# Performance work log

Hardware: AMD Instinct MI355X
Metric: run time of the kernel (lower is better)

The kernel has to match this reference:

```python
import jax, jax.numpy as jnp
import numpy as np

C = 128        # in_channels
HEADS = 4      # n_heads
GROUPS = 32    # GroupNorm groups
EPS = 1e-6
B, H, W = 1, 64, 64


def setup_inputs() -> dict:
    key = jax.random.key(0)
    ks = jax.random.split(key, 5)
    def w(k):
        return jax.random.normal(k, (C, C), jnp.float32) * 0.02
    return {
        "x": jax.random.normal(ks[0], (B, C, H, W), jnp.float32),
        "gn_gamma": jnp.ones((C,), jnp.float32),
        "gn_beta": jnp.zeros((C,), jnp.float32),
        "wq": w(ks[1]), "bq": jnp.zeros((C,), jnp.float32),
        "wk": w(ks[2]), "bk": jnp.zeros((C,), jnp.float32),
        "wv": w(ks[3]), "bv": jnp.zeros((C,), jnp.float32),
        "wp": w(ks[4]), "bp": jnp.zeros((C,), jnp.float32),
    }


def _group_norm(x, gamma, beta):
    b, c, h, w = x.shape
    xg = x.reshape(b, GROUPS, c // GROUPS, h, w)
    mu = xg.mean(axis=(2, 3, 4), keepdims=True)
    var = xg.var(axis=(2, 3, 4), keepdims=True)
    xn = ((xg - mu) * jax.lax.rsqrt(var + EPS)).reshape(b, c, h, w)
    return xn * gamma[None, :, None, None] + beta[None, :, None, None]


def _conv1x1(x, wgt, bias):
    # 1x1 conv == per-pixel channel matmul
    return jnp.einsum('bchw,oc->bohw', x, wgt) + bias[None, :, None, None]


def reference(x, gn_gamma, gn_beta, wq, bq, wk, bk, wv, bv, wp, bp):
    b, c, h, w = x.shape
    cph = c // HEADS  # channels per head
    xn = _group_norm(x, gn_gamma, gn_beta)
    q = _conv1x1(xn, wq, bq)
    k = _conv1x1(xn, wk, bk)
    v = _conv1x1(xn, wv, bv)

    # einops 'b (c heads) h w': heads is the INNER channel factor
    def split_ch(t):  # -> (b, heads, cph, h*w)
        return t.reshape(b, cph, HEADS, h * w).transpose(0, 2, 1, 3)

    qh = split_ch(q).transpose(0, 1, 3, 2)  # (b, heads, hw, cph)
    kh = split_ch(k)                          # (b, heads, cph, hw)
    vh = split_ch(v)                          # (b, heads, cph, hw)

    scale = c ** (-0.5)  # NOTE: full in_channels, as in the original code
    attn = jnp.einsum('bhic,bhcj->bhij', qh, kh) * scale  # (b, heads, hw, hw)
    attn = jax.nn.softmax(attn, axis=2)  # softmax over QUERY axis (dim=2), non-standard

    out = jnp.einsum('bhik,bhjk->bhji', attn, vh)  # (b, heads, cph, hw)
    # 'b heads c (h w) -> b (c heads) h w'
    out = out.reshape(b, HEADS, cph, h, w).transpose(0, 2, 1, 3, 4).reshape(b, c, h, w)
    return _conv1x1(out, wp, bp) + x
```

## Files before the change

### kernel.cpp

```cpp
#include <hip/hip_runtime.h>
#include <hip/hip_bf16.h>


#define HWSZ 4096
#define QSCALE2 0.12752649759422368f
#define QSPLIT 8
#define KSPLIT 8
#define EPS 1e-6f

typedef __bf16 bf16x8 __attribute__((ext_vector_type(8)));
typedef float f32x4 __attribute__((ext_vector_type(4)));

union FragU { uint4 u; bf16x8 v; };

#if __has_builtin(__builtin_amdgcn_exp2f)
#define EXP2F(x) __builtin_amdgcn_exp2f(x)
#else
#define EXP2F(x) exp2f(x)
#endif

__device__ __forceinline__ unsigned int pack_bf16(float lo, float hi) {
  unsigned int ul, uh;
  __builtin_memcpy(&ul, &lo, 4);
  __builtin_memcpy(&uh, &hi, 4);
  return __builtin_amdgcn_perm(uh + 0x8000u, ul + 0x8000u, 0x07060302u);
}

__global__ __launch_bounds__(256) void prep_kernel(
    const float* __restrict__ wq, const float* __restrict__ wk,
    const float* __restrict__ wv, const float* __restrict__ wp,
    const float* __restrict__ x, __hip_bfloat16* __restrict__ wb,
    float* __restrict__ gnpart) {
  int b = blockIdx.x, t = threadIdx.x;
  if (b < 64) {
    int m = b >> 4, chunk = b & 15;
    const float* src = (m == 0) ? wq : (m == 1) ? wk : (m == 2) ? wv : wp;
    float sc = (m == 0) ? QSCALE2 : 1.0f;
    int idx = chunk * 1024 + t * 4;
    float4 v = *reinterpret_cast<const float4*>(src + idx);
    uint2 st;
    st.x = pack_bf16(v.x * sc, v.y * sc);
    st.y = pack_bf16(v.z * sc, v.w * sc);
    *reinterpret_cast<uint2*>(wb + m * 16384 + idx) = st;
  } else {
    int ch = b - 64;
    const float4* x4 = reinterpret_cast<const float4*>(x + ch * HWSZ);
    float s = 0.f, ss = 0.f;
    for (int e = t; e < 1024; e += 256) {
      float4 v = x4[e];
      s += v.x + v.y + v.z + v.w;
      ss += v.x * v.x + v.y * v.y + v.z * v.z + v.w * v.w;
    }
    for (int off = 32; off; off >>= 1) {
      s += __shfl_down(s, off);
      ss += __shfl_down(ss, off);
    }
    __shared__ float rs[4], rss[4];
    int wid = t >> 6;
    if ((t & 63) == 0) { rs[wid] = s; rss[wid] = ss; }
    __syncthreads();
    if (t == 0) {
      gnpart[ch] = rs[0] + rs[1] + rs[2] + rs[3];
      gnpart[128 + ch] = rss[0] + rss[1] + rss[2] + rss[3];
    }
  }
}

__global__ __launch_bounds__(512) void qkv_mfma_kernel(
    const float* __restrict__ x, const float* __restrict__ gnpart,
    const float* __restrict__ gamma, const float* __restrict__ beta,
    const __hip_bfloat16* __restrict__ wb, const float* __restrict__ bq,
    const float* __restrict__ bk, const float* __restrict__ bv,
    __hip_bfloat16* __restrict__ qt, __hip_bfloat16* __restrict__ kt,
    __hip_bfloat16* __restrict__ vb) {
  __shared__ float stats_lds[32][2];
  __shared__ __align__(16) __hip_bfloat16 xnT[16][136];
  __shared__ __align__(16) __hip_bfloat16 qs_[4][16][40];
  __shared__ __align__(16) __hip_bfloat16 ks_[4][16][40];
  __shared__ __align__(16) __hip_bfloat16 vs_[128][24];
  int t = threadIdx.x;
  int p0 = blockIdx.x * 16;
  if (t < 32) {
    float s = 0.f, ss = 0.f;
#pragma unroll
    for (int q = 0; q < 4; ++q) {
      s += gnpart[t * 4 + q];
      ss += gnpart[128 + t * 4 + q];
    }
    float mu = s * (1.f / 16384.f);
    float var = ss * (1.f / 16384.f) - mu * mu;
    stats_lds[t][0] = mu;
    stats_lds[t][1] = rsqrtf(var + EPS);
  }
  __syncthreads();
#pragma unroll
  for (int e = t; e < 2048; e += 512) {
    int c = e >> 4, p = e & 15;
    int g = c >> 2;
    float xv = x[c * HWSZ + p0 + p];
    float xn = (xv - stats_lds[g][0]) * stats_lds[g][1] * gamma[c] + beta[c];
    xnT[p][c] = __float2bfloat16(xn);
  }
  __syncthreads();
  int lane = t & 63, w = t >> 6;
  int l15 = lane & 15, g = lane >> 4;
  FragU bfr[4];
#pragma unroll
  for (int kk = 0; kk < 4; ++kk)
    bfr[kk].u = *reinterpret_cast<const uint4*>(&xnT[l15][kk * 32 + 8 * g]);
  int o0 = w * 16;

#define DO_CONV(WMAT, BIAS, BSCALE, LDSW)                                        \
  {                                                                              \
    f32x4 bi = *reinterpret_cast<const f32x4*>((BIAS) + o0 + 4 * g);             \
    f32x4 acc = bi * (BSCALE);                                                   \
    _Pragma("unroll") for (int kk = 0; kk < 4; ++kk) {                           \
      FragU a;                                                                   \
      a.u = *reinterpret_cast<const uint4*>((WMAT) +                             \
            (o0 + l15) * 128 + kk * 32 + 8 * g);                                 \
      acc = __builtin_amdgcn_mfma_f32_16x16x32_bf16(a.v, bfr[kk].v, acc, 0, 0, 0); \
    }                                                                            \
    _Pragma("unroll") for (int r = 0; r < 4; ++r) {                              \
      int o = o0 + 4 * g + r;                                                    \
      LDSW;                                                                      \
    }                                                                            \
  }

  DO_CONV(wb, bq, QSCALE2, qs_[o & 3][l15][o >> 2] = __float2bfloat16(acc[r]))
  DO_CONV(wb + 16384, bk, 1.0f, ks_[o & 3][l15][o >> 2] = __float2bfloat16(acc[r]))
  DO_CONV(wb + 32768, bv, 1.0f, vs_[o][l15] = __float2bfloat16(acc[r]))
#undef DO_CONV
  __syncthreads();
  if (t < 256) {
    int row = t >> 2, ch = t & 3;
    int h = row >> 4, p = row & 15;
    uint4 vq = *reinterpret_cast<const uint4*>(&qs_[h][p][ch * 8]);
    *reinterpret_cast<uint4*>(qt + (h * HWSZ + p0 + p) * 32 + ch * 8) = vq;
  } else {
    int tt = t - 256;
    int row = tt >> 2, ch = tt & 3;
    int h = row >> 4, p = row & 15;
    uint4 vk = *reinterpret_cast<const uint4*>(&ks_[h][p][ch * 8]);
    *reinterpret_cast<uint4*>(kt + (h * HWSZ + p0 + p) * 32 + ch * 8) = vk;
  }
  if (t < 256) {
    int o = t >> 1, half = t & 1;
    uint4 vv = *reinterpret_cast<const uint4*>(&vs_[o][half * 8]);
    *reinterpret_cast<uint4*>(vb + o * HWSZ + p0 + half * 8) = vv;
  }
}

__global__ __launch_bounds__(256, 4) void colstats_kernel(
    const __hip_bfloat16* __restrict__ qt, const __hip_bfloat16* __restrict__ kt,
    float* __restrict__ colpart) {
  int h = blockIdx.y, t = threadIdx.x, qs = blockIdx.z;
  int w = t >> 6, lane = t & 63;
  int l15 = lane & 15, g = lane >> 4;
  int k0 = blockIdx.x * 256 + w * 64;
  FragU a[4];
#pragma unroll
  for (int u = 0; u < 4; ++u)
    a[u].u = *reinterpret_cast<const uint4*>(kt + (h * HWSZ + k0 + u * 16 + l15) * 32 + 8 * g);
  float l[4][4];
#pragma unroll
  for (int u = 0; u < 4; ++u)
#pragma unroll
    for (int r = 0; r < 4; ++r) l[u][r] = 0.f;
  const __hip_bfloat16* qbase =
      qt + h * HWSZ * 32 + (qs * (HWSZ / QSPLIT) + l15) * 32 + 8 * g;
  f32x4 z = {0.f, 0.f, 0.f, 0.f};
#pragma unroll 2
  for (int it = 0; it < HWSZ / QSPLIT / 16; ++it) {
    FragU b;
    b.u = *reinterpret_cast<const uint4*>(qbase + it * 512);
#pragma unroll
    for (int u = 0; u < 4; ++u) {
      f32x4 d = __builtin_amdgcn_mfma_f32_16x16x32_bf16(a[u].v, b.v, z, 0, 0, 0);
#pragma unroll
      for (int r = 0; r < 4; ++r) l[u][r] += EXP2F(d[r]);
    }
  }
#pragma unroll
  for (int off = 1; off < 16; off <<= 1)
#pragma unroll
    for (int u = 0; u < 4; ++u)
#pragma unroll
      for (int r = 0; r < 4; ++r) l[u][r] += __shfl_xor(l[u][r], off);
  if (l15 == 0) {
#pragma unroll
    for (int u = 0; u < 4; ++u)
#pragma unroll
      for (int r = 0; r < 4; ++r)
        colpart[(qs * 4 + h) * HWSZ + k0 + u * 16 + 4 * g + r] = l[u][r];
  }
}

__global__ __launch_bounds__(256) void wscale_kernel(
    const float* __restrict__ colpart, __hip_bfloat16* __restrict__ vb) {
  __shared__ float rlds[128];
  int b = blockIdx.x, t = threadIdx.x;
  int kr0 = b * 32;
  if (t < 128) {
    int h = t >> 5, k = kr0 + (t & 31);
    float s = 0.f;
#pragma unroll
    for (int qs = 0; qs < QSPLIT; ++qs) s += colpart[(qs * 4 + h) * HWSZ + k];
    rlds[t] = 1.0f / s;
  }
  __syncthreads();
  int row = t >> 1, koff = (t & 1) * 16;
  int h = row & 3;
  __hip_bfloat16* p = vb + row * HWSZ + kr0 + koff;
  FragU u0, u1;
  u0.u = *reinterpret_cast<const uint4*>(p);
  u1.u = *reinterpret_cast<const uint4*>(p + 8);
  const float* r = rlds + h * 32 + koff;
  float f[16];
#pragma unroll
  for (int j = 0; j < 8; ++j) {
    f[j] = (float)u0.v[j] * r[j];
    f[8 + j] = (float)u1.v[j] * r[8 + j];
  }
  uint4 s0, s1;
  s0.x = pack_bf16(f[0], f[1]);  s0.y = pack_bf16(f[2], f[3]);
  s0.z = pack_bf16(f[4], f[5]);  s0.w = pack_bf16(f[6], f[7]);
  s1.x = pack_bf16(f[8], f[9]);  s1.y = pack_bf16(f[10], f[11]);
  s1.z = pack_bf16(f[12], f[13]); s1.w = pack_bf16(f[14], f[15]);
  *reinterpret_cast<uint4*>(p) = s0;
  *reinterpret_cast<uint4*>(p + 8) = s1;
}

__global__ __launch_bounds__(256, 4) void attn_pv_kernel(
    const __hip_bfloat16* __restrict__ qt, const __hip_bfloat16* __restrict__ kt,
    const __hip_bfloat16* __restrict__ vb, __hip_bfloat16* __restrict__ aopb) {
  __shared__ __align__(16) char p_lds[4][2][2048];
  int h = blockIdx.y, t = threadIdx.x;
  int kc0 = blockIdx.z * (HWSZ / KSPLIT);
  int w = t >> 6, lane = t & 63;
  int l15 = lane & 15, g = lane >> 4;
  int swz = l15 & 7;
  int i0 = blockIdx.x * 128 + w * 32;
  FragU bq0, bq1;
  bq0.u = *reinterpret_cast<const uint4*>(qt + (h * HWSZ + i0 + l15) * 32 + 8 * g);
  bq1.u = *reinterpret_cast<const uint4*>(qt + (h * HWSZ + i0 + 16 + l15) * 32 + 8 * g);
  f32x4 zero4 = {0.f, 0.f, 0.f, 0.f};
  f32x4 acc[2][2];
#pragma unroll
  for (int q = 0; q < 2; ++q)
#pragma unroll
    for (int ch = 0; ch < 2; ++ch) acc[q][ch] = zero4;
  __hip_bfloat16* ao = aopb + blockIdx.z * (128 * HWSZ);
#pragma unroll 2
  for (int k0 = kc0; k0 < kc0 + HWSZ / KSPLIT; k0 += 64) {
    FragU a[4];
#pragma unroll
    for (int kt4 = 0; kt4 < 4; ++kt4)
      a[kt4].u = *reinterpret_cast<const uint4*>(
          kt + (h * HWSZ + k0 + kt4 * 16 + l15) * 32 + 8 * g);
    FragU bvf[2][2];
#pragma unroll
    for (int ks = 0; ks < 2; ++ks)
#pragma unroll
      for (int ch = 0; ch < 2; ++ch)
        bvf[ks][ch].u = *reinterpret_cast<const uint4*>(
            vb + ((l15 + 16 * ch) * 4 + h) * HWSZ + k0 + ks * 32 + 8 * g);
    f32x4 st[2][4];
#pragma unroll
    for (int kt4 = 0; kt4 < 4; ++kt4) {
      st[0][kt4] = __builtin_amdgcn_mfma_f32_16x16x32_bf16(a[kt4].v, bq0.v, zero4, 0, 0, 0);
      st[1][kt4] = __builtin_amdgcn_mfma_f32_16x16x32_bf16(a[kt4].v, bq1.v, zero4, 0, 0, 0);
    }
#pragma unroll
    for (int q = 0; q < 2; ++q) {
      char* pw = p_lds[w][q];
#pragma unroll
      for (int kt4 = 0; kt4 < 4; ++kt4) {
        uint2 pk;
        pk.x = pack_bf16(EXP2F(st[q][kt4][0]), EXP2F(st[q][kt4][1]));
        pk.y = pack_bf16(EXP2F(st[q][kt4][2]), EXP2F(st[q][kt4][3]));
        int c8 = kt4 * 4 + g;
        int byte_w = l15 * 128 + ((((c8 >> 1) ^ swz)) << 4) + ((c8 & 1) << 3);
        *reinterpret_cast<uint2*>(pw + byte_w) = pk;
      }
    }
#pragma unroll
    for (int q = 0; q < 2; ++q) {
      char* pw = p_lds[w][q];
#pragma unroll
      for (int ks = 0; ks < 2; ++ks) {
        FragU ap;
        int byte_r = l15 * 128 + (((ks * 4 + g) ^ swz) << 4);
        ap.u = *reinterpret_cast<const uint4*>(pw + byte_r);
#pragma unroll
        for (int ch = 0; ch < 2; ++ch)
          acc[q][ch] = __builtin_amdgcn_mfma_f32_16x16x32_bf16(ap.v, bvf[ks][ch].v,
                                                               acc[q][ch], 0, 0, 0);
      }
    }
  }
#pragma unroll
  for (int q = 0; q < 2; ++q)
#pragma unroll
    for (int ch = 0; ch < 2; ++ch) {
      uint2 pk;
      pk.x = pack_bf16(acc[q][ch][0], acc[q][ch][1]);
      pk.y = pack_bf16(acc[q][ch][2], acc[q][ch][3]);
      *reinterpret_cast<uint2*>(
          ao + ((l15 + 16 * ch) * 4 + h) * HWSZ + i0 + q * 16 + 4 * g) = pk;
    }
}

__global__ __launch_bounds__(512) void proj_mfma_kernel(
    const __hip_bfloat16* __restrict__ aopb, const __hip_bfloat16* __restrict__ wpb,
    const float* __restrict__ bp, const float* __restrict__ x,
    float* __restrict__ out) {
  __shared__ __align__(16) __hip_bfloat16 aoT[16][136];
  __shared__ __align__(16) float obuf[128][20];
  int t = threadIdx.x;
  int p0 = blockIdx.x * 16;
  if (t < 256) {
    int c = t >> 1, half = t & 1;
    float s[8];
#pragma unroll
    for (int j = 0; j < 8; ++j) s[j] = 0.f;
#pragma unroll
    for (int z = 0; z < KSPLIT; ++z) {
      FragU u;
      u.u = *reinterpret_cast<const uint4*>(aopb + z * (128 * HWSZ) + c * HWSZ + p0 + half * 8);
#pragma unroll
      for (int j = 0; j < 8; ++j) s[j] += (float)u.v[j];
    }
#pragma unroll
    for (int j = 0; j < 8; ++j) aoT[half * 8 + j][c] = __float2bfloat16(s[j]);
  }
  __syncthreads();
  int lane = t & 63, w = t >> 6;
  int l15 = lane & 15, g = lane >> 4;
  FragU bfr[4];
#pragma unroll
  for (int kk = 0; kk < 4; ++kk)
    bfr[kk].u = *reinterpret_cast<const uint4*>(&aoT[l15][kk * 32 + 8 * g]);
  int o0 = w * 16;
  f32x4 acc = *reinterpret_cast<const f32x4*>(bp + o0 + 4 * g);
#pragma unroll
  for (int kk = 0; kk < 4; ++kk) {
    FragU a;
    a.u = *reinterpret_cast<const uint4*>(wpb + (o0 + l15) * 128 + kk * 32 + 8 * g);
    acc = __builtin_amdgcn_mfma_f32_16x16x32_bf16(a.v, bfr[kk].v, acc, 0, 0, 0);
  }
#pragma unroll
  for (int r = 0; r < 4; ++r) obuf[o0 + 4 * g + r][l15] = acc[r];
  __syncthreads();
  int row = t >> 2, ch = t & 3;
  float4 o4 = *reinterpret_cast<const float4*>(&obuf[row][ch * 4]);
  float4 xv = *reinterpret_cast<const float4*>(x + row * HWSZ + p0 + ch * 4);
  float4 rr = {o4.x + xv.x, o4.y + xv.y, o4.z + xv.z, o4.w + xv.w};
  *reinterpret_cast<float4*>(out + row * HWSZ + p0 + ch * 4) = rr;
}

extern "C" void kernel_launch(void* const* d_in, const int* in_sizes, int n_in,
                              void* d_out, int out_size, void* d_ws, size_t ws_size,
                              hipStream_t stream) {
  const float* x = (const float*)d_in[0];
  const float* gamma = (const float*)d_in[1];
  const float* beta = (const float*)d_in[2];
  const float* wq = (const float*)d_in[3];
  const float* bq = (const float*)d_in[4];
  const float* wk = (const float*)d_in[5];
  const float* bk = (const float*)d_in[6];
  const float* wv = (const float*)d_in[7];
  const float* bv = (const float*)d_in[8];
  const float* wp = (const float*)d_in[9];
  const float* bp = (const float*)d_in[10];
  float* out = (float*)d_out;

  char* ws = (char*)d_ws;
  __hip_bfloat16* qt = (__hip_bfloat16*)(ws);
  __hip_bfloat16* kt = (__hip_bfloat16*)(ws + (1 << 20));
  __hip_bfloat16* vb = (__hip_bfloat16*)(ws + (2 << 20));
  __hip_bfloat16* aopb = (__hip_bfloat16*)(ws + (3 << 20));
  char* tail = ws + ((3 + KSPLIT) << 20);
  float* colpart = (float*)(tail);
  __hip_bfloat16* wb = (__hip_bfloat16*)(tail + (512 << 10));
  float* gnpart = (float*)(tail + (640 << 10));

  prep_kernel<<<192, 256, 0, stream>>>(wq, wk, wv, wp, x, wb, gnpart);
  qkv_mfma_kernel<<<256, 512, 0, stream>>>(x, gnpart, gamma, beta, wb, bq, bk, bv,
                                           qt, kt, vb);
  colstats_kernel<<<dim3(16, 4, QSPLIT), 256, 0, stream>>>(qt, kt, colpart);
  wscale_kernel<<<128, 256, 0, stream>>>(colpart, vb);
  attn_pv_kernel<<<dim3(32, 4, KSPLIT), 256, 0, stream>>>(qt, kt, vb, aopb);
  proj_mfma_kernel<<<256, 512, 0, stream>>>(aopb, wb + 49152, bp, x, out);
}
```

Measured before the change: 64.36 us.

## Fold column-softmax normalization into attn_pv via log-sum bias and widen query tiles

Drops the separate wscale kernel that rescaled V by the reciprocal column sums. Each attn_pv block now sums the colpart partials for its key chunk, stores -log2(sum) in LDS, and feeds it as the MFMA accumulator init, so the normalization happens inside the exp2. Each wave also covers 64 queries instead of 32, halving the grid and reusing K/V fragments across more queries. The cost is higher register and LDS use (launch bounds drop to 2) and the colpart reduction repeated by every query block.

```diff
diff --git a/kernel.cpp b/kernel.cpp
--- a/kernel.cpp
+++ b/kernel.cpp
@@ -109,7 +109,6 @@
   for (int kk = 0; kk < 4; ++kk)
     bfr[kk].u = *reinterpret_cast<const uint4*>(&xnT[l15][kk * 32 + 8 * g]);
   int o0 = w * 16;
-
 #define DO_CONV(WMAT, BIAS, BSCALE, LDSW)                                        \
   {                                                                              \
     f32x4 bi = *reinterpret_cast<const f32x4*>((BIAS) + o0 + 4 * g);             \
@@ -125,7 +124,6 @@
       LDSW;                                                                      \
     }                                                                            \
   }
-
   DO_CONV(wb, bq, QSCALE2, qs_[o & 3][l15][o >> 2] = __float2bfloat16(acc[r]))
   DO_CONV(wb + 16384, bk, 1.0f, ks_[o & 3][l15][o >> 2] = __float2bfloat16(acc[r]))
   DO_CONV(wb + 32768, bv, 1.0f, vs_[o][l15] = __float2bfloat16(acc[r]))
@@ -195,68 +193,46 @@
   }
 }
 
-__global__ __launch_bounds__(256) void wscale_kernel(
-    const float* __restrict__ colpart, __hip_bfloat16* __restrict__ vb) {
-  __shared__ float rlds[128];
-  int b = blockIdx.x, t = threadIdx.x;
-  int kr0 = b * 32;
-  if (t < 128) {
-    int h = t >> 5, k = kr0 + (t & 31);
-    float s = 0.f;
-#pragma unroll
-    for (int qs = 0; qs < QSPLIT; ++qs) s += colpart[(qs * 4 + h) * HWSZ + k];
-    rlds[t] = 1.0f / s;
-  }
-  __syncthreads();
-  int row = t >> 1, koff = (t & 1) * 16;
-  int h = row & 3;
-  __hip_bfloat16* p = vb + row * HWSZ + kr0 + koff;
-  FragU u0, u1;
-  u0.u = *reinterpret_cast<const uint4*>(p);
-  u1.u = *reinterpret_cast<const uint4*>(p + 8);
-  const float* r = rlds + h * 32 + koff;
-  float f[16];
-#pragma unroll
-  for (int j = 0; j < 8; ++j) {
-    f[j] = (float)u0.v[j] * r[j];
-    f[8 + j] = (float)u1.v[j] * r[8 + j];
-  }
-  uint4 s0, s1;
-  s0.x = pack_bf16(f[0], f[1]);  s0.y = pack_bf16(f[2], f[3]);
-  s0.z = pack_bf16(f[4], f[5]);  s0.w = pack_bf16(f[6], f[7]);
-  s1.x = pack_bf16(f[8], f[9]);  s1.y = pack_bf16(f[10], f[11]);
-  s1.z = pack_bf16(f[12], f[13]); s1.w = pack_bf16(f[14], f[15]);
-  *reinterpret_cast<uint4*>(p) = s0;
-  *reinterpret_cast<uint4*>(p + 8) = s1;
-}
-
-__global__ __launch_bounds__(256, 4) void attn_pv_kernel(
+__global__ __launch_bounds__(256, 2) void attn_pv_kernel(
     const __hip_bfloat16* __restrict__ qt, const __hip_bfloat16* __restrict__ kt,
-    const __hip_bfloat16* __restrict__ vb, __hip_bfloat16* __restrict__ aopb) {
-  __shared__ __align__(16) char p_lds[4][2][2048];
+    const __hip_bfloat16* __restrict__ vb, const float* __restrict__ colpart,
+    __hip_bfloat16* __restrict__ aopb) {
+  __shared__ __align__(16) char p_lds[4][4][2048];
+  __shared__ float c2_lds[HWSZ / KSPLIT];
   int h = blockIdx.y, t = threadIdx.x;
   int kc0 = blockIdx.z * (HWSZ / KSPLIT);
+#pragma unroll
+  for (int e = t; e < HWSZ / KSPLIT; e += 256) {
+    float s = 0.f;
+#pragma unroll
+    for (int qs = 0; qs < QSPLIT; ++qs) s += colpart[(qs * 4 + h) * HWSZ + kc0 + e];
+    c2_lds[e] = -__log2f(s);
+  }
+  __syncthreads();
   int w = t >> 6, lane = t & 63;
   int l15 = lane & 15, g = lane >> 4;
   int swz = l15 & 7;
-  int i0 = blockIdx.x * 128 + w * 32;
-  FragU bq0, bq1;
-  bq0.u = *reinterpret_cast<const uint4*>(qt + (h * HWSZ + i0 + l15) * 32 + 8 * g);
-  bq1.u = *reinterpret_cast<const uint4*>(qt + (h * HWSZ + i0 + 16 + l15) * 32 + 8 * g);
-  f32x4 zero4 = {0.f, 0.f, 0.f, 0.f};
-  f32x4 acc[2][2];
-#pragma unroll
-  for (int q = 0; q < 2; ++q)
-#pragma unroll
-    for (int ch = 0; ch < 2; ++ch) acc[q][ch] = zero4;
+  int i0 = blockIdx.x * 256 + w * 64;
+  FragU bq[4];
+#pragma unroll
+  for (int qs = 0; qs < 4; ++qs)
+    bq[qs].u = *reinterpret_cast<const uint4*>(
+        qt + (h * HWSZ + i0 + qs * 16 + l15) * 32 + 8 * g);
+  f32x4 acc[4][2];
+#pragma unroll
+  for (int qs = 0; qs < 4; ++qs)
+#pragma unroll
+    for (int ch = 0; ch < 2; ++ch) acc[qs][ch] = (f32x4){0.f, 0.f, 0.f, 0.f};
   __hip_bfloat16* ao = aopb + blockIdx.z * (128 * HWSZ);
-#pragma unroll 2
   for (int k0 = kc0; k0 < kc0 + HWSZ / KSPLIT; k0 += 64) {
     FragU a[4];
-#pragma unroll
-    for (int kt4 = 0; kt4 < 4; ++kt4)
+    f32x4 c2[4];
+#pragma unroll
+    for (int kt4 = 0; kt4 < 4; ++kt4) {
       a[kt4].u = *reinterpret_cast<const uint4*>(
           kt + (h * HWSZ + k0 + kt4 * 16 + l15) * 32 + 8 * g);
+      c2[kt4] = *reinterpret_cast<const f32x4*>(c2_lds + (k0 - kc0) + kt4 * 16 + 4 * g);
+    }
     FragU bvf[2][2];
 #pragma unroll
     for (int ks = 0; ks < 2; ++ks)
@@ -264,28 +240,23 @@
       for (int ch = 0; ch < 2; ++ch)
         bvf[ks][ch].u = *reinterpret_cast<const uint4*>(
             vb + ((l15 + 16 * ch) * 4 + h) * HWSZ + k0 + ks * 32 + 8 * g);
-    f32x4 st[2][4];
-#pragma unroll
-    for (int kt4 = 0; kt4 < 4; ++kt4) {
-      st[0][kt4] = __builtin_amdgcn_mfma_f32_16x16x32_bf16(a[kt4].v, bq0.v, zero4, 0, 0, 0);
-      st[1][kt4] = __builtin_amdgcn_mfma_f32_16x16x32_bf16(a[kt4].v, bq1.v, zero4, 0, 0, 0);
-    }
-#pragma unroll
-    for (int q = 0; q < 2; ++q) {
-      char* pw = p_lds[w][q];
+#pragma unroll
+    for (int qs = 0; qs < 4; ++qs) {
+      f32x4 st[4];
+#pragma unroll
+      for (int kt4 = 0; kt4 < 4; ++kt4)
+        st[kt4] = __builtin_amdgcn_mfma_f32_16x16x32_bf16(a[kt4].v, bq[qs].v,
+                                                          c2[kt4], 0, 0, 0);
+      char* pw = p_lds[w][qs];
 #pragma unroll
       for (int kt4 = 0; kt4 < 4; ++kt4) {
         uint2 pk;
-        pk.x = pack_bf16(EXP2F(st[q][kt4][0]), EXP2F(st[q][kt4][1]));
-        pk.y = pack_bf16(EXP2F(st[q][kt4][2]), EXP2F(st[q][kt4][3]));
+        pk.x = pack_bf16(EXP2F(st[kt4][0]), EXP2F(st[kt4][1]));
+        pk.y = pack_bf16(EXP2F(st[kt4][2]), EXP2F(st[kt4][3]));
         int c8 = kt4 * 4 + g;
         int byte_w = l15 * 128 + ((((c8 >> 1) ^ swz)) << 4) + ((c8 & 1) << 3);
         *reinterpret_cast<uint2*>(pw + byte_w) = pk;
       }
-    }
-#pragma unroll
-    for (int q = 0; q < 2; ++q) {
-      char* pw = p_lds[w][q];
 #pragma unroll
       for (int ks = 0; ks < 2; ++ks) {
         FragU ap;
@@ -293,20 +264,20 @@
         ap.u = *reinterpret_cast<const uint4*>(pw + byte_r);
 #pragma unroll
         for (int ch = 0; ch < 2; ++ch)
-          acc[q][ch] = __builtin_amdgcn_mfma_f32_16x16x32_bf16(ap.v, bvf[ks][ch].v,
-                                                               acc[q][ch], 0, 0, 0);
+          acc[qs][ch] = __builtin_amdgcn_mfma_f32_16x16x32_bf16(
+              ap.v, bvf[ks][ch].v, acc[qs][ch], 0, 0, 0);
       }
     }
   }
 #pragma unroll
-  for (int q = 0; q < 2; ++q)
+  for (int qs = 0; qs < 4; ++qs)
 #pragma unroll
     for (int ch = 0; ch < 2; ++ch) {
       uint2 pk;
-      pk.x = pack_bf16(acc[q][ch][0], acc[q][ch][1]);
-      pk.y = pack_bf16(acc[q][ch][2], acc[q][ch][3]);
+      pk.x = pack_bf16(acc[qs][ch][0], acc[qs][ch][1]);
+      pk.y = pack_bf16(acc[qs][ch][2], acc[qs][ch][3]);
       *reinterpret_cast<uint2*>(
-          ao + ((l15 + 16 * ch) * 4 + h) * HWSZ + i0 + q * 16 + 4 * g) = pk;
+          ao + ((l15 + 16 * ch) * 4 + h) * HWSZ + i0 + qs * 16 + 4 * g) = pk;
     }
 }
 
@@ -388,7 +359,6 @@
   qkv_mfma_kernel<<<256, 512, 0, stream>>>(x, gnpart, gamma, beta, wb, bq, bk, bv,
                                            qt, kt, vb);
   colstats_kernel<<<dim3(16, 4, QSPLIT), 256, 0, stream>>>(qt, kt, colpart);
-  wscale_kernel<<<128, 256, 0, stream>>>(colpart, vb);
-  attn_pv_kernel<<<dim3(32, 4, KSPLIT), 256, 0, stream>>>(qt, kt, vb, aopb);
+  attn_pv_kernel<<<dim3(16, 4, KSPLIT), 256, 0, stream>>>(qt, kt, vb, colpart, aopb);
   proj_mfma_kernel<<<256, 512, 0, stream>>>(aopb, wb + 49152, bp, x, out);
 }
```

Result: faster. 52.99 us (-17.7%).
